# Optimization experiments

Hardware: AMD Instinct MI355X
Metric: run time of the kernel (lower is better)

Reference implementation:

```python
import jax, jax.numpy as jnp
import numpy as np

V, E, H = 50000, 512, 1024
HD = H // 2            # per-direction LSTM hidden
T = 2048               # sequence length
TAGS, START, STOP = 32, 30, 31
NEG = -10000.0


def setup_inputs() -> dict:
    key = jax.random.key(0)
    ks = jax.random.split(key, 14)
    s = 1.0 / np.sqrt(HD)
    u = lambda k, shape: jax.random.uniform(k, shape, jnp.float32, -s, s)
    sentence = jax.random.randint(ks[0], (T,), 0, V)
    emb = jax.random.normal(ks[1], (V, E), jnp.float32)
    # PyTorch LSTM gate layout: [i, f, g, o] stacked along dim 0
    w_ih_f, w_hh_f, b_f = u(ks[2], (4 * HD, E)), u(ks[3], (4 * HD, HD)), u(ks[4], (4 * HD,))
    w_ih_b, w_hh_b, b_b = u(ks[5], (4 * HD, E)), u(ks[6], (4 * HD, HD)), u(ks[7], (4 * HD,))
    W_out = u(ks[8], (TAGS, H))
    b_out = u(ks[9], (TAGS,))
    transitions = jax.random.normal(ks[10], (TAGS, TAGS), jnp.float32)
    transitions = transitions.at[START, :].set(NEG).at[:, STOP].set(NEG)
    h0 = jax.random.normal(ks[11], (2, HD), jnp.float32)  # [dir, HD], batch=1 squeezed
    c0 = jax.random.normal(ks[12], (2, HD), jnp.float32)
    return dict(sentence=sentence, emb=emb, w_ih_f=w_ih_f, w_hh_f=w_hh_f, b_f=b_f,
                w_ih_b=w_ih_b, w_hh_b=w_hh_b, b_b=b_b, W_out=W_out, b_out=b_out,
                transitions=transitions, h0=h0, c0=c0)


def _lstm_dir(x, h0, c0, w_ih, w_hh, b, reverse):
    # x: [T, E]; single-sequence LSTM scan, gates ordered i,f,g,o as in torch
    xg = x @ w_ih.T + b  # [T, 4*HD], precompute input contribution
    def step(carry, xt):
        h, c = carry
        g = xt + w_hh @ h
        i, f, gg, o = jnp.split(g, 4)
        c = jax.nn.sigmoid(f) * c + jax.nn.sigmoid(i) * jnp.tanh(gg)
        h = jax.nn.sigmoid(o) * jnp.tanh(c)
        return (h, c), h
    _, hs = jax.lax.scan(step, (h0, c0), xg, reverse=reverse)
    return hs  # [T, HD]


def _viterbi(feats, transitions):
    # feats: [T, TAGS]
    init = jnp.full((TAGS,), NEG, feats.dtype).at[START].set(0.0)
    def step(fv, feat):
        scores = fv[None, :] + transitions       # [next, prev]
        bp = jnp.argmax(scores, axis=1)          # [TAGS]
        fv_new = jnp.max(scores, axis=1) + feat
        return fv_new, bp
    fv, bps = jax.lax.scan(step, init, feats)
    terminal = fv + transitions[STOP]
    best = jnp.argmax(terminal)
    score = terminal[best]
    def back(tag, bp):
        return bp[tag], tag
    _, path = jax.lax.scan(back, best, bps, reverse=True)
    return score, path  # path: [T] int tags


def reference(sentence, emb, w_ih_f, w_hh_f, b_f, w_ih_b, w_hh_b, b_b,
              W_out, b_out, transitions, h0, c0):
    x = emb[sentence]  # [T, E]
    hf = _lstm_dir(x, h0[0], c0[0], w_ih_f, w_hh_f, b_f, reverse=False)
    hb = _lstm_dir(x, h0[1], c0[1], w_ih_b, w_hh_b, b_b, reverse=True)
    feats = jnp.concatenate([hf, hb], axis=-1) @ W_out.T + b_out  # [T, TAGS]
    score, path = _viterbi(feats, transitions)
    return score, path
```

## Files before the change

### kernel.cpp

```cpp
#include <hip/hip_runtime.h>
#include <math.h>

#define TT 2048
#define EE 512
#define HDD 512
#define TAGS 32
#define STARTT 30
#define STOPP 31
#define NEGV -10000.0f
#define VCH 256
#define SENT 0xFFFFFFFFu

__device__ __forceinline__ float fsig(float x) {
    return __builtin_amdgcn_rcpf(1.f + __expf(-x));
}
__device__ __forceinline__ float ftanh(float x) {
    return 2.f * __builtin_amdgcn_rcpf(1.f + __expf(-2.f * x)) - 1.f;
}
__device__ __forceinline__ void waitflag(const int* f) {
    while (__hip_atomic_load(f, __ATOMIC_ACQUIRE, __HIP_MEMORY_SCOPE_AGENT) < 32)
        __builtin_amdgcn_s_sleep(1);
}

__global__ __launch_bounds__(256, 2) void k_main(
        const int* __restrict__ sent, const float* __restrict__ emb,
        const float* __restrict__ wihf, const float* __restrict__ whhf,
        const float* __restrict__ bfv,
        const float* __restrict__ wihb, const float* __restrict__ whhb,
        const float* __restrict__ bbv,
        const float* __restrict__ h0, const float* __restrict__ c0,
        float* __restrict__ xg, float* __restrict__ hs,
        int* __restrict__ xflag) {
    const int tid = threadIdx.x;

    if (blockIdx.x >= 128) {
        const int gid  = blockIdx.x - 128;
        const int gy   = gid >> 5;
        const int jj   = gy >> 1;
        const int dir  = gy & 1;
        const int tile = dir ? (31 - jj) : jj;
        const float* __restrict__ w    = dir ? wihb : wihf;
        const float* __restrict__ bias = dir ? bbv : bfv;
        const int tb = tile * 64;
        const int nb = (gid & 31) * 64;
        __shared__ float As[64][17];
        __shared__ float Bs[64][17];
        const int lr = tid >> 2;
        const int lc = (tid & 3) * 4;
        const int ty = tid >> 4;
        const int tx = tid & 15;
        const int sidx = sent[tb + lr];
        float acc[4][4] = {};
        for (int k0 = 0; k0 < EE; k0 += 16) {
            float4 av = *(const float4*)(emb + (size_t)sidx * EE + k0 + lc);
            float4 bv = *(const float4*)(w + (size_t)(nb + lr) * EE + k0 + lc);
            As[lr][lc+0] = av.x; As[lr][lc+1] = av.y; As[lr][lc+2] = av.z; As[lr][lc+3] = av.w;
            Bs[lr][lc+0] = bv.x; Bs[lr][lc+1] = bv.y; Bs[lr][lc+2] = bv.z; Bs[lr][lc+3] = bv.w;
            __syncthreads();
            #pragma unroll
            for (int kk = 0; kk < 16; ++kk) {
                float a[4], b[4];
                #pragma unroll
                for (int i = 0; i < 4; ++i) a[i] = As[ty*4+i][kk];
                #pragma unroll
                for (int j = 0; j < 4; ++j) b[j] = Bs[tx*4+j][kk];
                #pragma unroll
                for (int i = 0; i < 4; ++i)
                    #pragma unroll
                    for (int j = 0; j < 4; ++j)
                        acc[i][j] += a[i] * b[j];
            }
            __syncthreads();
        }
        #pragma unroll
        for (int i = 0; i < 4; ++i) {
            float4 o;
            o.x = acc[i][0] + bias[nb + tx*4 + 0];
            o.y = acc[i][1] + bias[nb + tx*4 + 1];
            o.z = acc[i][2] + bias[nb + tx*4 + 2];
            o.w = acc[i][3] + bias[nb + tx*4 + 3];
            *(float4*)(xg + ((size_t)dir*TT + tb + ty*4 + i) * 2048 + nb + tx*4) = o;
        }
        __syncthreads();
        if (tid == 0)
            __hip_atomic_fetch_add(&xflag[dir * 32 + tile], 1,
                                   __ATOMIC_RELEASE, __HIP_MEMORY_SCOPE_AGENT);
        return;
    }

    const int wg  = blockIdx.x & 63;
    const int dir = blockIdx.x >> 6;
    const float* __restrict__ whh = dir ? whhb : whhf;
    const int lane   = tid & 63;
    const int waveid = tid >> 6;
    const int unit   = lane >> 5;
    const int gate   = (lane >> 3) & 3;
    const int seg    = lane & 7;
    const int hidx   = (wg * 4 + waveid) * 2 + unit;
    const int grow   = gate * HDD + hidx;

    float4 w[16];
    {
        const float4* wp = (const float4*)(whh + (size_t)grow * HDD + seg * 64);
        #pragma unroll
        for (int i = 0; i < 16; ++i) w[i] = wp[i];
    }

    __shared__ float hbuf[2][528];

    float c = c0[dir * HDD + hidx];

    const int* flags = xflag + dir * 32;
    const int t0 = dir ? (TT - 1) : 0;
    int curtile = t0 >> 6;
    waitflag(&flags[curtile]);
    float xvn = __uint_as_float(__hip_atomic_load(
        (const unsigned*)(xg + ((size_t)dir * TT + t0) * 2048 + grow),
        __ATOMIC_RELAXED, __HIP_MEMORY_SCOPE_AGENT));

    const int g0 = 2 * tid;
    const int soff = (g0 >> 7) * 132 + (g0 & 127);
    hbuf[0][soff]     = h0[dir * HDD + g0];
    hbuf[0][soff + 1] = h0[dir * HDD + g0 + 1];

    for (int s = 0; s < TT; ++s) {
        const int t = dir ? (TT - 1 - s) : s;
        const float xv = xvn;
        if (s + 1 < TT) {
            const int tn = dir ? (TT - 2 - s) : (s + 1);
            const int tilen = tn >> 6;
            if (tilen != curtile) { waitflag(&flags[tilen]); curtile = tilen; }
            xvn = __uint_as_float(__hip_atomic_load(
                (const unsigned*)(xg + ((size_t)dir * TT + tn) * 2048 + grow),
                __ATOMIC_RELAXED, __HIP_MEMORY_SCOPE_AGENT));
        }

        float* hb = hbuf[s & 1];
        if (s > 0) {
            const int tprev = dir ? (t + 1) : (t - 1);
            const unsigned long long* hsrc = (const unsigned long long*)
                (hs + ((size_t)dir * TT + tprev) * HDD) + tid;
            unsigned long long vv = __hip_atomic_load(hsrc,
                    __ATOMIC_RELAXED, __HIP_MEMORY_SCOPE_AGENT);
            while ((unsigned)vv == SENT || (unsigned)(vv >> 32) == SENT)
                vv = __hip_atomic_load(hsrc,
                        __ATOMIC_RELAXED, __HIP_MEMORY_SCOPE_AGENT);
            hb[soff]     = __uint_as_float((unsigned)vv);
            hb[soff + 1] = __uint_as_float((unsigned)(vv >> 32));
        }
        __syncthreads();

        const float4* hp = (const float4*)(hb + (seg >> 1) * 132 + (seg & 1) * 64);
        float a0 = 0.f, a1 = 0.f, a2 = 0.f, a3 = 0.f;
        #pragma unroll
        for (int i = 0; i < 16; i += 4) {
            float4 h0v = hp[i], h1v = hp[i+1], h2v = hp[i+2], h3v = hp[i+3];
            a0 += w[i  ].x*h0v.x + w[i  ].y*h0v.y + w[i  ].z*h0v.z + w[i  ].w*h0v.w;
            a1 += w[i+1].x*h1v.x + w[i+1].y*h1v.y + w[i+1].z*h1v.z + w[i+1].w*h1v.w;
            a2 += w[i+2].x*h2v.x + w[i+2].y*h2v.y + w[i+2].z*h2v.z + w[i+2].w*h2v.w;
            a3 += w[i+3].x*h3v.x + w[i+3].y*h3v.y + w[i+3].z*h3v.z + w[i+3].w*h3v.w;
        }
        float acc = (a0 + a1) + (a2 + a3);
        acc += __shfl_xor(acc, 1);
        acc += __shfl_xor(acc, 2);
        acc += __shfl_xor(acc, 4);
        acc += xv;

        const int base = lane & ~31;
        const float iv = __shfl(acc, base + 0);
        const float fv = __shfl(acc, base + 8);
        const float gv = __shfl(acc, base + 16);
        const float ov = __shfl(acc, base + 24);
        c = fsig(fv) * c + fsig(iv) * ftanh(gv);
        const float h = fsig(ov) * ftanh(c);

        if ((lane & 31) == 0)
            __hip_atomic_store(&hs[((size_t)dir * TT + t) * HDD + hidx], h,
                               __ATOMIC_RELAXED, __HIP_MEMORY_SCOPE_AGENT);
    }
}

__global__ __launch_bounds__(256) void k_feats(const float* __restrict__ hs,
        const float* __restrict__ Wout, const float* __restrict__ bout,
        float* __restrict__ feats) {
    const int t = blockIdx.x;
    const int tid = threadIdx.x;
    const int tag = tid >> 3;
    const int chunk = tid & 7;
    const float* __restrict__ hrow = (chunk < 4)
        ? hs + (size_t)t * HDD
        : hs + ((size_t)TT + t) * HDD - 512;
    float acc = 0.f;
    const float4* wp = (const float4*)(Wout + (size_t)tag * 1024 + chunk * 128);
    const float4* hp = (const float4*)(hrow + chunk * 128);
    #pragma unroll
    for (int i = 0; i < 32; ++i) {
        float4 wv = wp[i];
        float4 hv = hp[i];
        acc += wv.x*hv.x + wv.y*hv.y + wv.z*hv.z + wv.w*hv.w;
    }
    __shared__ float red[TAGS][9];
    red[tag][chunk] = acc;
    __syncthreads();
    if (tid < TAGS) {
        float s = bout[tid];
        #pragma unroll
        for (int c = 0; c < 8; ++c) s += red[tid][c];
        feats[(size_t)t * TAGS + tid] = s;
    }
}

__global__ __launch_bounds__(64) void k_viterbi(const float* __restrict__ feats,
        const float* __restrict__ trans, float* __restrict__ out) {
    const int lane = threadIdx.x;
    const int n  = lane & 31;
    const int ph = lane >> 5;
    __shared__ float fvs[TAGS];
    __shared__ unsigned char bp[TT][TAGS];
    __shared__ __align__(16) float fbuf[VCH * TAGS];
    float tr[16];
    #pragma unroll
    for (int p = 0; p < 16; ++p) tr[p] = trans[n * TAGS + ph * 16 + p];
    if (lane < TAGS) fvs[lane] = (lane == STARTT) ? 0.f : NEGV;
    __syncthreads();
    for (int c0 = 0; c0 < TT; c0 += VCH) {
        const float4* src = (const float4*)(feats + (size_t)c0 * TAGS);
        float4* dst = (float4*)fbuf;
        for (int i = lane; i < VCH * TAGS / 4; i += 64) dst[i] = src[i];
        __syncthreads();
        for (int lt = 0; lt < VCH; ++lt) {
            const int t = c0 + lt;
            float bv = fvs[ph * 16] + tr[0];
            int bi = ph * 16;
            #pragma unroll
            for (int p = 1; p < 16; ++p) {
                const float cand = fvs[ph * 16 + p] + tr[p];
                if (cand > bv) { bv = cand; bi = ph * 16 + p; }
            }
            const float obv = __shfl_xor(bv, 32);
            const int   obi = __shfl_xor(bi, 32);
            if (obv > bv || (obv == bv && obi < bi)) { bv = obv; bi = obi; }
            const float nf = bv + fbuf[lt * TAGS + n];
            if (ph == 0) bp[t][n] = (unsigned char)bi;
            __syncthreads();
            if (ph == 0) fvs[n] = nf;
            __syncthreads();
        }
    }
    if (lane < TAGS) fvs[lane] += trans[STOPP * TAGS + lane];
    __syncthreads();
    if (lane == 0) {
        float bs = fvs[0]; int best = 0;
        for (int i = 1; i < TAGS; ++i)
            if (fvs[i] > bs) { bs = fvs[i]; best = i; }
        out[0] = bs;
        int tag = best;
        for (int t = TT - 1; t >= 0; --t) {
            out[1 + t] = (float)tag;
            tag = bp[t][tag];
        }
    }
}

extern "C" void kernel_launch(void* const* d_in, const int* in_sizes, int n_in,
                              void* d_out, int out_size, void* d_ws, size_t ws_size,
                              hipStream_t stream) {
    const int*   sent  = (const int*)  d_in[0];
    const float* emb   = (const float*)d_in[1];
    const float* wihf  = (const float*)d_in[2];
    const float* whhf  = (const float*)d_in[3];
    const float* bfv   = (const float*)d_in[4];
    const float* wihb  = (const float*)d_in[5];
    const float* whhb  = (const float*)d_in[6];
    const float* bbv   = (const float*)d_in[7];
    const float* Wout  = (const float*)d_in[8];
    const float* bout  = (const float*)d_in[9];
    const float* trans = (const float*)d_in[10];
    const float* h0    = (const float*)d_in[11];
    const float* c0    = (const float*)d_in[12];
    float* out = (float*)d_out;

    char* ws = (char*)d_ws;
    float* xg    = (float*)(ws + ((size_t)4  << 20));
    float* hs    = (float*)(ws + ((size_t)36 << 20));
    float* feats = (float*)(ws + ((size_t)44 << 20));
    int* xflag   = (int*)  (ws + ((size_t)44 << 20) + (320u << 10));

    hipMemsetAsync(hs, 0xFF, (size_t)2 * TT * HDD * sizeof(float), stream);
    hipMemsetAsync(xflag, 0, 64 * sizeof(int), stream);
    k_main   <<<dim3(128 + 2048), 256, 0, stream>>>(sent, emb, wihf, whhf, bfv,
                                                    wihb, whhb, bbv, h0, c0,
                                                    xg, hs, xflag);
    k_feats  <<<TT, 256, 0, stream>>>(hs, Wout, bout, feats);
    k_viterbi<<<1, 64, 0, stream>>>(feats, trans, out);
}
```

Measured before the change: 4.154 ms.

## Spread LSTM recurrence over twice as many blocks, tree-reduce Viterbi argmax

```diff
diff --git a/kernel.cpp b/kernel.cpp
--- a/kernel.cpp
+++ b/kernel.cpp
@@ -33,8 +33,8 @@
         int* __restrict__ xflag) {
     const int tid = threadIdx.x;
 
-    if (blockIdx.x >= 128) {
-        const int gid  = blockIdx.x - 128;
+    if (blockIdx.x >= 256) {
+        const int gid  = blockIdx.x - 256;
         const int gy   = gid >> 5;
         const int jj   = gy >> 1;
         const int dir  = gy & 1;
@@ -88,25 +88,24 @@
         return;
     }
 
-    const int wg  = blockIdx.x & 63;
-    const int dir = blockIdx.x >> 6;
+    const int wg  = blockIdx.x & 127;
+    const int dir = blockIdx.x >> 7;
     const float* __restrict__ whh = dir ? whhb : whhf;
     const int lane   = tid & 63;
     const int waveid = tid >> 6;
-    const int unit   = lane >> 5;
-    const int gate   = (lane >> 3) & 3;
-    const int seg    = lane & 7;
-    const int hidx   = (wg * 4 + waveid) * 2 + unit;
+    const int gate   = lane >> 4;
+    const int seg    = lane & 15;
+    const int hidx   = wg * 4 + waveid;
     const int grow   = gate * HDD + hidx;
 
-    float4 w[16];
+    float4 w[8];
     {
-        const float4* wp = (const float4*)(whh + (size_t)grow * HDD + seg * 64);
+        const float4* wp = (const float4*)(whh + (size_t)grow * HDD + seg * 32);
         #pragma unroll
-        for (int i = 0; i < 16; ++i) w[i] = wp[i];
-    }
-
-    __shared__ float hbuf[2][528];
+        for (int i = 0; i < 8; ++i) w[i] = wp[i];
+    }
+
+    __shared__ float hbuf[2][576];
 
     float c = c0[dir * HDD + hidx];
 
@@ -119,7 +118,7 @@
         __ATOMIC_RELAXED, __HIP_MEMORY_SCOPE_AGENT));
 
     const int g0 = 2 * tid;
-    const int soff = (g0 >> 7) * 132 + (g0 & 127);
+    const int soff = (g0 >> 5) * 36 + (g0 & 31);
     hbuf[0][soff]     = h0[dir * HDD + g0];
     hbuf[0][soff + 1] = h0[dir * HDD + g0 + 1];
 
@@ -150,31 +149,36 @@
         }
         __syncthreads();
 
-        const float4* hp = (const float4*)(hb + (seg >> 1) * 132 + (seg & 1) * 64);
+        const float4* hp = (const float4*)(hb + seg * 36);
         float a0 = 0.f, a1 = 0.f, a2 = 0.f, a3 = 0.f;
-        #pragma unroll
-        for (int i = 0; i < 16; i += 4) {
-            float4 h0v = hp[i], h1v = hp[i+1], h2v = hp[i+2], h3v = hp[i+3];
-            a0 += w[i  ].x*h0v.x + w[i  ].y*h0v.y + w[i  ].z*h0v.z + w[i  ].w*h0v.w;
-            a1 += w[i+1].x*h1v.x + w[i+1].y*h1v.y + w[i+1].z*h1v.z + w[i+1].w*h1v.w;
-            a2 += w[i+2].x*h2v.x + w[i+2].y*h2v.y + w[i+2].z*h2v.z + w[i+2].w*h2v.w;
-            a3 += w[i+3].x*h3v.x + w[i+3].y*h3v.y + w[i+3].z*h3v.z + w[i+3].w*h3v.w;
+        {
+            float4 h0v = hp[0], h1v = hp[1], h2v = hp[2], h3v = hp[3];
+            a0 += w[0].x*h0v.x + w[0].y*h0v.y + w[0].z*h0v.z + w[0].w*h0v.w;
+            a1 += w[1].x*h1v.x + w[1].y*h1v.y + w[1].z*h1v.z + w[1].w*h1v.w;
+            a2 += w[2].x*h2v.x + w[2].y*h2v.y + w[2].z*h2v.z + w[2].w*h2v.w;
+            a3 += w[3].x*h3v.x + w[3].y*h3v.y + w[3].z*h3v.z + w[3].w*h3v.w;
+            float4 h4v = hp[4], h5v = hp[5], h6v = hp[6], h7v = hp[7];
+            a0 += w[4].x*h4v.x + w[4].y*h4v.y + w[4].z*h4v.z + w[4].w*h4v.w;
+            a1 += w[5].x*h5v.x + w[5].y*h5v.y + w[5].z*h5v.z + w[5].w*h5v.w;
+            a2 += w[6].x*h6v.x + w[6].y*h6v.y + w[6].z*h6v.z + w[6].w*h6v.w;
+            a3 += w[7].x*h7v.x + w[7].y*h7v.y + w[7].z*h7v.z + w[7].w*h7v.w;
         }
         float acc = (a0 + a1) + (a2 + a3);
         acc += __shfl_xor(acc, 1);
         acc += __shfl_xor(acc, 2);
         acc += __shfl_xor(acc, 4);
+        acc += __shfl_xor(acc, 8);
         acc += xv;
 
-        const int base = lane & ~31;
-        const float iv = __shfl(acc, base + 0);
-        const float fv = __shfl(acc, base + 8);
-        const float gv = __shfl(acc, base + 16);
-        const float ov = __shfl(acc, base + 24);
-        c = fsig(fv) * c + fsig(iv) * ftanh(gv);
-        const float h = fsig(ov) * ftanh(c);
-
-        if ((lane & 31) == 0)
+        const float act = (gate == 2) ? ftanh(acc) : fsig(acc);
+        const float ia = __shfl(act, 0);
+        const float fa = __shfl(act, 16);
+        const float ga = __shfl(act, 32);
+        const float oa = __shfl(act, 48);
+        c = fa * c + ia * ga;
+        const float h = oa * ftanh(c);
+
+        if (lane == 0)
             __hip_atomic_store(&hs[((size_t)dir * TT + t) * HDD + hidx], h,
                                __ATOMIC_RELAXED, __HIP_MEMORY_SCOPE_AGENT);
     }
@@ -230,13 +234,31 @@
         __syncthreads();
         for (int lt = 0; lt < VCH; ++lt) {
             const int t = c0 + lt;
-            float bv = fvs[ph * 16] + tr[0];
-            int bi = ph * 16;
+            float v0[8]; int i0[8];
             #pragma unroll
-            for (int p = 1; p < 16; ++p) {
-                const float cand = fvs[ph * 16 + p] + tr[p];
-                if (cand > bv) { bv = cand; bi = ph * 16 + p; }
+            for (int j = 0; j < 8; ++j) {
+                const float a = fvs[ph * 16 + 2*j]     + tr[2*j];
+                const float b = fvs[ph * 16 + 2*j + 1] + tr[2*j + 1];
+                const bool gt = b > a;
+                v0[j] = gt ? b : a; i0[j] = gt ? 2*j + 1 : 2*j;
             }
+            float v1[4]; int i1[4];
+            #pragma unroll
+            for (int j = 0; j < 4; ++j) {
+                const bool gt = v0[2*j + 1] > v0[2*j];
+                v1[j] = gt ? v0[2*j + 1] : v0[2*j];
+                i1[j] = gt ? i0[2*j + 1] : i0[2*j];
+            }
+            float v2[2]; int i2[2];
+            #pragma unroll
+            for (int j = 0; j < 2; ++j) {
+                const bool gt = v1[2*j + 1] > v1[2*j];
+                v2[j] = gt ? v1[2*j + 1] : v1[2*j];
+                i2[j] = gt ? i1[2*j + 1] : i1[2*j];
+            }
+            const bool gt = v2[1] > v2[0];
+            float bv = gt ? v2[1] : v2[0];
+            int   bi = ph * 16 + (gt ? i2[1] : i2[0]);
             const float obv = __shfl_xor(bv, 32);
             const int   obi = __shfl_xor(bi, 32);
             if (obv > bv || (obv == bv && obi < bi)) { bv = obv; bi = obi; }
@@ -288,7 +310,7 @@
 
     hipMemsetAsync(hs, 0xFF, (size_t)2 * TT * HDD * sizeof(float), stream);
     hipMemsetAsync(xflag, 0, 64 * sizeof(int), stream);
-    k_main   <<<dim3(128 + 2048), 256, 0, stream>>>(sent, emb, wihf, whhf, bfv,
+    k_main   <<<dim3(256 + 2048), 256, 0, stream>>>(sent, emb, wihf, whhf, bfv,
                                                     wihb, whhb, bbv, h0, c0,
                                                     xg, hs, xflag);
     k_feats  <<<TT, 256, 0, stream>>>(hs, Wout, bout, feats);
```

Result: slower. 5.535 ms (+33.2%).
